# Performance work log

Measured on AMD Instinct MI355X. Metric: run time of the kernel, lower is better.

## Reference

```python
import jax, jax.numpy as jnp
import numpy as np

B, S, D, H = 4, 1024, 1024, 16
HD = D // H
EPS = 1e-5


def setup_inputs() -> dict:
    key = jax.random.key(0)
    ks = jax.random.split(key, 12)
    sc = 0.02
    return {
        "x": jax.random.normal(ks[0], (B, S, D), jnp.float32),
        "WQ": jax.random.normal(ks[1], (D, D), jnp.float32) * sc,
        "WK": jax.random.normal(ks[2], (D, D), jnp.float32) * sc,
        "WV": jax.random.normal(ks[3], (D, D), jnp.float32) * sc,
        "Wo": jax.random.normal(ks[4], (D, D), jnp.float32) * sc,
        "bo": jnp.zeros((D,), jnp.float32),
        "W1": jax.random.normal(ks[5], (D, 4 * D), jnp.float32) * sc,
        "b1": jnp.zeros((4 * D,), jnp.float32),
        "W2": jax.random.normal(ks[6], (4 * D, D), jnp.float32) * sc,
        "b2": jnp.zeros((D,), jnp.float32),
        "ln1_s": jnp.ones((D,), jnp.float32),
        "ln1_b": jnp.zeros((D,), jnp.float32),
        "ln2_s": jnp.ones((D,), jnp.float32),
        "ln2_b": jnp.zeros((D,), jnp.float32),
    }


def _layernorm(x, scale, shift):
    mean = jnp.mean(x, axis=-1, keepdims=True)
    var = jnp.mean((x - mean) ** 2, axis=-1, keepdims=True)  # unbiased=False
    return scale * ((x - mean) / jnp.sqrt(var + EPS)) + shift


def _gelu(x):
    c = jnp.sqrt(2.0 / jnp.pi).astype(x.dtype)
    return 0.5 * x * (1.0 + jnp.tanh(c * (x + 0.044715 * x ** 3)))


def reference(x, WQ, WK, WV, Wo, bo, W1, b1, W2, b2, ln1_s, ln1_b, ln2_s, ln2_b):
    b, s, d = x.shape
    # --- attention sub-block (pre-norm) ---
    h = _layernorm(x, ln1_s, ln1_b)
    q = (h @ WQ).reshape(b, s, H, HD).transpose(0, 2, 1, 3)  # [B,H,S,HD]
    k = (h @ WK).reshape(b, s, H, HD).transpose(0, 2, 1, 3)
    v = (h @ WV).reshape(b, s, H, HD).transpose(0, 2, 1, 3)
    scores = jnp.einsum("bhqd,bhkd->bhqk", q, k)
    causal = jnp.triu(jnp.ones((s, s), dtype=bool), k=1)
    scores = jnp.where(causal, -jnp.inf, scores)
    attn = jax.nn.softmax(scores / jnp.sqrt(jnp.float32(HD)), axis=-1)
    ctx = jnp.einsum("bhqk,bhkd->bhqd", attn, v)
    ctx = ctx.transpose(0, 2, 1, 3).reshape(b, s, d)
    x = x + (ctx @ Wo + bo)
    # --- FF sub-block (pre-norm) ---
    h = _layernorm(x, ln2_s, ln2_b)
    h = _gelu(h @ W1 + b1)
    return x + (h @ W2 + b2)
```

## Files before the change

### kernel.cpp

```cpp
#include <hip/hip_runtime.h>
#include <hip/hip_bf16.h>

#define DIM   1024
#define NHEAD 16
#define HDIM  64
#define BATCH 4
#define SEQ   1024
#define MTOT  (BATCH*SEQ)
#define DFF   (4*DIM)
#define LDQ   3072

typedef _Float16 f16x8 __attribute__((ext_vector_type(8)));
typedef _Float16 f16x4 __attribute__((ext_vector_type(4)));
typedef float    f32x4 __attribute__((ext_vector_type(4)));

__device__ __forceinline__ float geluf(float x) {
    float x3 = x * x * x;
    return 0.5f * x * (1.0f + tanhf(0.7978845608028654f * (x + 0.044715f * x3)));
}

__device__ __forceinline__ int swz_off(int row, int slot) {
    return row * 128 + ((slot ^ (row & 7)) << 4);
}
__device__ __forceinline__ f16x8 ldsfrag(const _Float16* s, int row, int slot) {
    return *(const f16x8*)((const char*)s + swz_off(row, slot));
}

template <int NCHUNK>
__device__ __forceinline__ void stage_async(const _Float16* __restrict__ g, int ld,
                                            _Float16* s, int w, int lane) {
    int r_in = lane >> 3;
    int sslot = lane & 7;
    int lslot = sslot ^ r_in;
#pragma unroll
    for (int q = 0; q < NCHUNK; ++q) {
        int chunk = w * NCHUNK + q;
        int row = chunk * 8 + r_in;
        const _Float16* gp = g + (size_t)row * ld + lslot * 8;
        _Float16* sp = s + chunk * 512;
        __builtin_amdgcn_global_load_lds(
            (const __attribute__((address_space(1))) void*)gp,
            (__attribute__((address_space(3))) void*)sp, 16, 0, 0);
    }
}

__global__ __launch_bounds__(256) void k_tcvt(const float* __restrict__ src,
                                              _Float16* __restrict__ dst,
                                              int K, int N) {
    __shared__ float tile[32][33];
    int n0 = blockIdx.x * 32, k0 = blockIdx.y * 32;
    int tx = threadIdx.x, ty = threadIdx.y;
#pragma unroll
    for (int i = 0; i < 32; i += 8)
        tile[ty + i][tx] = src[(size_t)(k0 + ty + i) * N + (n0 + tx)];
    __syncthreads();
#pragma unroll
    for (int i = 0; i < 32; i += 8)
        dst[(size_t)(n0 + ty + i) * K + (k0 + tx)] = (_Float16)tile[tx][ty + i];
}

__global__ __launch_bounds__(256) void k_tcvt3(const float* __restrict__ s0,
                                               const float* __restrict__ s1,
                                               const float* __restrict__ s2,
                                               _Float16* __restrict__ dst) {
    __shared__ float tile[32][33];
    const float* src = blockIdx.z == 0 ? s0 : (blockIdx.z == 1 ? s1 : s2);
    _Float16* d = dst + (size_t)blockIdx.z * (1024 * 1024);
    int n0 = blockIdx.x * 32, k0 = blockIdx.y * 32;
    int tx = threadIdx.x, ty = threadIdx.y;
#pragma unroll
    for (int i = 0; i < 32; i += 8)
        tile[ty + i][tx] = src[(size_t)(k0 + ty + i) * 1024 + (n0 + tx)];
    __syncthreads();
#pragma unroll
    for (int i = 0; i < 32; i += 8)
        d[(size_t)(n0 + ty + i) * 1024 + (k0 + tx)] = (_Float16)tile[tx][ty + i];
}

__global__ __launch_bounds__(256) void k_ln(const float* __restrict__ x,
                                            const float* __restrict__ sc,
                                            const float* __restrict__ sh,
                                            _Float16* __restrict__ out) {
    int row = blockIdx.x;
    int t = threadIdx.x;
    float4 v = ((const float4*)(x + (size_t)row * DIM))[t];
    float sum = v.x + v.y + v.z + v.w;
    float sq  = v.x * v.x + v.y * v.y + v.z * v.z + v.w * v.w;
#pragma unroll
    for (int m = 1; m < 64; m <<= 1) {
        sum += __shfl_xor(sum, m);
        sq  += __shfl_xor(sq, m);
    }
    __shared__ float rs[4], rq[4];
    int w = t >> 6;
    if ((t & 63) == 0) { rs[w] = sum; rq[w] = sq; }
    __syncthreads();
    sum = rs[0] + rs[1] + rs[2] + rs[3];
    sq  = rq[0] + rq[1] + rq[2] + rq[3];
    float mean = sum * (1.0f / DIM);
    float var  = sq * (1.0f / DIM) - mean * mean;
    float rstd = rsqrtf(var + 1e-5f);
    float4 s4 = ((const float4*)sc)[t];
    float4 b4 = ((const float4*)sh)[t];
    f16x4 o;
    o[0] = (_Float16)(s4.x * ((v.x - mean) * rstd) + b4.x);
    o[1] = (_Float16)(s4.y * ((v.y - mean) * rstd) + b4.y);
    o[2] = (_Float16)(s4.z * ((v.z - mean) * rstd) + b4.z);
    o[3] = (_Float16)(s4.w * ((v.w - mean) * rstd) + b4.w);
    ((f16x4*)(out + (size_t)row * DIM))[t] = o;
}

template <int EPI>
__global__ __launch_bounds__(256) void k_gemm(const _Float16* __restrict__ A,
                                              const _Float16* __restrict__ BT,
                                              int M, int N, int K,
                                              _Float16* __restrict__ Ch,
                                              const float* __restrict__ bias) {
    __shared__ _Float16 As[128 * 64];
    __shared__ _Float16 Bs[128 * 64];
    int t = threadIdx.x;
    int m0 = blockIdx.y * 128, n0 = blockIdx.x * 128;
    int lane = t & 63, w = t >> 6;
    int wm = (w >> 1) * 64, wn = (w & 1) * 64;
    int lr = lane & 15, lg = lane >> 4;
    f32x4 acc[4][4];
#pragma unroll
    for (int i = 0; i < 4; ++i)
#pragma unroll
        for (int j = 0; j < 4; ++j) acc[i][j] = (f32x4){0.f, 0.f, 0.f, 0.f};

    const _Float16* Ag = A  + (size_t)m0 * K;
    const _Float16* Bg = BT + (size_t)n0 * K;
    for (int k0 = 0; k0 < K; k0 += 64) {
        stage_async<4>(Ag + k0, K, As, w, lane);
        stage_async<4>(Bg + k0, K, Bs, w, lane);
        __syncthreads();
#pragma unroll
        for (int kk = 0; kk < 2; ++kk) {
            f16x8 a[4], b[4];
#pragma unroll
            for (int i = 0; i < 4; ++i) a[i] = ldsfrag(As, wm + i * 16 + lr, kk * 4 + lg);
#pragma unroll
            for (int j = 0; j < 4; ++j) b[j] = ldsfrag(Bs, wn + j * 16 + lr, kk * 4 + lg);
#pragma unroll
            for (int i = 0; i < 4; ++i)
#pragma unroll
                for (int j = 0; j < 4; ++j)
                    acc[i][j] = __builtin_amdgcn_mfma_f32_16x16x32_f16(a[i], b[j], acc[i][j], 0, 0, 0);
        }
        __syncthreads();
    }
#pragma unroll
    for (int i = 0; i < 4; ++i) {
#pragma unroll
        for (int j = 0; j < 4; ++j) {
            int row = m0 + wm + i * 16 + lg * 4;
            int col = n0 + wn + j * 16 + lr;
#pragma unroll
            for (int r = 0; r < 4; ++r) {
                float v = acc[i][j][r];
                size_t idx = (size_t)(row + r) * N + col;
                if constexpr (EPI == 0) Ch[idx] = (_Float16)v;
                else                    Ch[idx] = (_Float16)geluf(v + bias[col]);
            }
        }
    }
}

__global__ __launch_bounds__(256) void k_gemm64(const _Float16* __restrict__ A,
                                                const _Float16* __restrict__ BT,
                                                int M, int N, int K,
                                                float* __restrict__ Cf,
                                                const float* __restrict__ bias,
                                                const float* __restrict__ resid) {
    __shared__ _Float16 As[128 * 64];
    __shared__ _Float16 Bs[64 * 64];
    int t = threadIdx.x;
    int m0 = blockIdx.y * 128, n0 = blockIdx.x * 64;
    int lane = t & 63, w = t >> 6;
    int wm = w * 32;
    int lr = lane & 15, lg = lane >> 4;
    f32x4 acc[2][4];
#pragma unroll
    for (int i = 0; i < 2; ++i)
#pragma unroll
        for (int j = 0; j < 4; ++j) acc[i][j] = (f32x4){0.f, 0.f, 0.f, 0.f};

    const _Float16* Ag = A  + (size_t)m0 * K;
    const _Float16* Bg = BT + (size_t)n0 * K;
    for (int k0 = 0; k0 < K; k0 += 64) {
        stage_async<4>(Ag + k0, K, As, w, lane);
        stage_async<2>(Bg + k0, K, Bs, w, lane);
        __syncthreads();
#pragma unroll
        for (int kk = 0; kk < 2; ++kk) {
            f16x8 a[2], b[4];
#pragma unroll
            for (int i = 0; i < 2; ++i) a[i] = ldsfrag(As, wm + i * 16 + lr, kk * 4 + lg);
#pragma unroll
            for (int j = 0; j < 4; ++j) b[j] = ldsfrag(Bs, j * 16 + lr, kk * 4 + lg);
#pragma unroll
            for (int i = 0; i < 2; ++i)
#pragma unroll
                for (int j = 0; j < 4; ++j)
                    acc[i][j] = __builtin_amdgcn_mfma_f32_16x16x32_f16(a[i], b[j], acc[i][j], 0, 0, 0);
        }
        __syncthreads();
    }
#pragma unroll
    for (int i = 0; i < 2; ++i) {
#pragma unroll
        for (int j = 0; j < 4; ++j) {
            int row = m0 + wm + i * 16 + lg * 4;
            int col = n0 + j * 16 + lr;
#pragma unroll
            for (int r = 0; r < 4; ++r) {
                size_t idx = (size_t)(row + r) * N + col;
                Cf[idx] = acc[i][j][r] + bias[col] + resid[idx];
            }
        }
    }
}

__global__ __launch_bounds__(64) void k_attn(const _Float16* __restrict__ QKV,
                                             _Float16* __restrict__ Og) {
    __shared__ _Float16 Vt[64 * 64];
    __shared__ _Float16 Ps[32 * 64];
    int lane = threadIdx.x;
    int id = blockIdx.x;
    int bh = id & 63;
    int qt = (SEQ / 32 - 1) - (id >> 6);
    int h = bh & 15, b = bh >> 4;
    int q0 = qt * 32;
    int lr = lane & 15, lg = lane >> 4;
    size_t base = (size_t)b * SEQ;
    int cq = h * HDIM, ck = 1024 + h * HDIM, cv = 2048 + h * HDIM;

    f16x8 aq[2][2];
#pragma unroll
    for (int i = 0; i < 2; ++i)
#pragma unroll
        for (int kk = 0; kk < 2; ++kk) {
            f16x8 v = *(const f16x8*)(QKV + (base + q0 + i * 16 + lr) * LDQ + cq + kk * 32 + lg * 8);
#pragma unroll
            for (int e = 0; e < 8; ++e) v[e] = v[e] * (_Float16)0.125f;
            aq[i][kk] = v;
        }

    f32x4 cacc[2][4];
#pragma unroll
    for (int i = 0; i < 2; ++i)
#pragma unroll
        for (int j = 0; j < 4; ++j) cacc[i][j] = (f32x4){0.f, 0.f, 0.f, 0.f};
    float mrun[2][4], lrun[2][4];
#pragma unroll
    for (int i = 0; i < 2; ++i)
#pragma unroll
        for (int r = 0; r < 4; ++r) { mrun[i][r] = -1e30f; lrun[i][r] = 0.f; }

    int ntiles = q0 / 64 + 1;
    for (int kt = 0; kt < ntiles; ++kt) {
        int k0 = kt * 64;
        {
            const _Float16* vr = QKV + (base + k0 + lane) * LDQ + cv;
            int kslot = lane >> 3;
            int kb2 = (lane & 7) * 2;
#pragma unroll
            for (int part = 0; part < 8; ++part) {
                f16x8 v8 = *(const f16x8*)(vr + part * 8);
#pragma unroll
                for (int e = 0; e < 8; ++e) {
                    int d = part * 8 + e;
                    *(_Float16*)((char*)Vt + d * 128 + ((kslot ^ (d & 7)) << 4) + kb2) = v8[e];
                }
            }
        }
        f32x4 sacc[2][4];
#pragma unroll
        for (int i = 0; i < 2; ++i)
#pragma unroll
            for (int j = 0; j < 4; ++j) sacc[i][j] = (f32x4){0.f, 0.f, 0.f, 0.f};
#pragma unroll
        for (int kk = 0; kk < 2; ++kk) {
            f16x8 bk[4];
#pragma unroll
            for (int j = 0; j < 4; ++j)
                bk[j] = *(const f16x8*)(QKV + (base + k0 + j * 16 + lr) * LDQ + ck + kk * 32 + lg * 8);
            __builtin_amdgcn_s_setprio(1);
#pragma unroll
            for (int i = 0; i < 2; ++i)
#pragma unroll
                for (int j = 0; j < 4; ++j)
                    sacc[i][j] = __builtin_amdgcn_mfma_f32_16x16x32_f16(aq[i][kk], bk[j], sacc[i][j], 0, 0, 0);
            __builtin_amdgcn_s_setprio(0);
        }
        if (kt == ntiles - 1) {
#pragma unroll
            for (int i = 0; i < 2; ++i)
#pragma unroll
                for (int j = 0; j < 4; ++j)
#pragma unroll
                    for (int r = 0; r < 4; ++r) {
                        int qq = q0 + i * 16 + lg * 4 + r;
                        int kc = k0 + j * 16 + lr;
                        if (kc > qq) sacc[i][j][r] = -1e30f;
                    }
        }
#pragma unroll
        for (int i = 0; i < 2; ++i) {
            float mn[4], al[4];
#pragma unroll
            for (int r = 0; r < 4; ++r) {
                float tm = fmaxf(fmaxf(sacc[i][0][r], sacc[i][1][r]),
                                 fmaxf(sacc[i][2][r], sacc[i][3][r]));
#pragma unroll
                for (int msk = 1; msk < 16; msk <<= 1) tm = fmaxf(tm, __shfl_xor(tm, msk));
                float m2 = fmaxf(mrun[i][r], tm);
                al[r] = __expf(mrun[i][r] - m2);
                mrun[i][r] = m2;
                mn[r] = m2;
            }
#pragma unroll
            for (int jd = 0; jd < 4; ++jd)
#pragma unroll
                for (int r = 0; r < 4; ++r) cacc[i][jd][r] *= al[r];
#pragma unroll
            for (int r = 0; r < 4; ++r) {
                float ps = 0.f;
#pragma unroll
                for (int j = 0; j < 4; ++j) {
                    float p = __expf(sacc[i][j][r] - mn[r]);
                    sacc[i][j][r] = p;
                    ps += p;
                }
#pragma unroll
                for (int msk = 1; msk < 16; msk <<= 1) ps += __shfl_xor(ps, msk);
                lrun[i][r] = lrun[i][r] * al[r] + ps;
            }
        }
#pragma unroll
        for (int i = 0; i < 2; ++i)
#pragma unroll
            for (int j = 0; j < 4; ++j) {
                int kc = j * 16 + lr;
                int ks = kc >> 3;
                int kb = (kc & 7) * 2;
#pragma unroll
                for (int r = 0; r < 4; ++r) {
                    int qq = i * 16 + lg * 4 + r;
                    *(_Float16*)((char*)Ps + qq * 128 + ((ks ^ (qq & 7)) << 4) + kb) =
                        (_Float16)sacc[i][j][r];
                }
            }
#pragma unroll
        for (int kk = 0; kk < 2; ++kk) {
            f16x8 pa[2], bv[4];
#pragma unroll
            for (int i = 0; i < 2; ++i)   pa[i]  = ldsfrag(Ps, i * 16 + lr,  kk * 4 + lg);
#pragma unroll
            for (int jd = 0; jd < 4; ++jd) bv[jd] = ldsfrag(Vt, jd * 16 + lr, kk * 4 + lg);
            __builtin_amdgcn_s_setprio(1);
#pragma unroll
            for (int i = 0; i < 2; ++i)
#pragma unroll
                for (int jd = 0; jd < 4; ++jd)
                    cacc[i][jd] = __builtin_amdgcn_mfma_f32_16x16x32_f16(pa[i], bv[jd], cacc[i][jd], 0, 0, 0);
            __builtin_amdgcn_s_setprio(0);
        }
    }
#pragma unroll
    for (int i = 0; i < 2; ++i)
#pragma unroll
        for (int jd = 0; jd < 4; ++jd)
#pragma unroll
            for (int r = 0; r < 4; ++r) {
                int qq = q0 + i * 16 + lg * 4 + r;
                int d = h * HDIM + jd * 16 + lr;
                Og[(base + qq) * DIM + d] = (_Float16)(cacc[i][jd][r] / lrun[i][r]);
            }
}

extern "C" void kernel_launch(void* const* d_in, const int* in_sizes, int n_in,
                              void* d_out, int out_size, void* d_ws, size_t ws_size,
                              hipStream_t stream) {
    const float* x    = (const float*)d_in[0];
    const float* WQ   = (const float*)d_in[1];
    const float* WK   = (const float*)d_in[2];
    const float* WV   = (const float*)d_in[3];
    const float* Wo   = (const float*)d_in[4];
    const float* bo   = (const float*)d_in[5];
    const float* W1   = (const float*)d_in[6];
    const float* b1   = (const float*)d_in[7];
    const float* W2   = (const float*)d_in[8];
    const float* b2   = (const float*)d_in[9];
    const float* ln1s = (const float*)d_in[10];
    const float* ln1b = (const float*)d_in[11];
    const float* ln2s = (const float*)d_in[12];
    const float* ln2b = (const float*)d_in[13];
    float* out = (float*)d_out;
    char* ws = (char*)d_ws;
    const size_t MB = 1024 * 1024;
    _Float16* WTqkv = (_Float16*)(ws + 0 * MB);
    _Float16* WTo   = (_Float16*)(ws + 6 * MB);
    _Float16* WT1   = (_Float16*)(ws + 8 * MB);
    _Float16* WT2   = (_Float16*)(ws + 16 * MB);
    _Float16* h1    = (_Float16*)(ws + 24 * MB);
    _Float16* qkvb  = (_Float16*)(ws + 32 * MB);
    _Float16* ctx   = (_Float16*)(ws + 56 * MB);
    _Float16* h2    = (_Float16*)(ws + 64 * MB);
    _Float16* ff1   = (_Float16*)(ws + 72 * MB);
    float*    x2    = (float*)   (ws + 104 * MB);

    dim3 tb(32, 8);
    k_tcvt3<<<dim3(32, 32, 3), tb, 0, stream>>>(WQ, WK, WV, WTqkv);
    k_tcvt<<<dim3(32, 32), tb, 0, stream>>>(Wo, WTo, 1024, 1024);
    k_tcvt<<<dim3(128, 32), tb, 0, stream>>>(W1, WT1, 1024, 4096);
    k_tcvt<<<dim3(32, 128), tb, 0, stream>>>(W2, WT2, 4096, 1024);

    k_ln<<<MTOT, 256, 0, stream>>>(x, ln1s, ln1b, h1);

    k_gemm<0><<<dim3(24, 32), 256, 0, stream>>>(h1, WTqkv, MTOT, LDQ, DIM, qkvb, nullptr);

    k_attn<<<dim3(2048), 64, 0, stream>>>(qkvb, ctx);

    k_gemm64<<<dim3(16, 32), 256, 0, stream>>>(ctx, WTo, MTOT, DIM, DIM, x2, bo, x);

    k_ln<<<MTOT, 256, 0, stream>>>(x2, ln2s, ln2b, h2);

    k_gemm<1><<<dim3(32, 32), 256, 0, stream>>>(h2, WT1, MTOT, DFF, DIM, ff1, b1);

    k_gemm64<<<dim3(16, 32), 256, 0, stream>>>(ff1, WT2, MTOT, DIM, DFF, out, b2, x2);
}
```

Baseline: 258.5 us.

## Double-buffer GEMM LDS tiles, raise MFMA priority, use exp-based GELU

Both GEMM kernels now keep two LDS buffers, so the async load of the next K-tile is issued before the MFMAs on the current tile run, and only one barrier remains per iteration. The aim is to hide global-to-LDS latency behind matrix math. s_setprio raises wave priority around the MFMA block. GELU is rewritten as x*sigmoid(2z), using __expf and a hardware reciprocal instead of tanhf. The cost is double the LDS per block, which may lower occupancy, plus slightly reduced GELU precision.

```diff
diff --git a/kernel.cpp b/kernel.cpp
--- a/kernel.cpp
+++ b/kernel.cpp
@@ -15,8 +15,8 @@
 typedef float    f32x4 __attribute__((ext_vector_type(4)));
 
 __device__ __forceinline__ float geluf(float x) {
-    float x3 = x * x * x;
-    return 0.5f * x * (1.0f + tanhf(0.7978845608028654f * (x + 0.044715f * x3)));
+    float z2 = 1.5957691216057308f * (x + 0.044715f * x * x * x);
+    return x * __builtin_amdgcn_rcpf(1.0f + __expf(-z2));
 }
 
 __device__ __forceinline__ int swz_off(int row, int slot) {
@@ -116,8 +116,8 @@
                                               int M, int N, int K,
                                               _Float16* __restrict__ Ch,
                                               const float* __restrict__ bias) {
-    __shared__ _Float16 As[128 * 64];
-    __shared__ _Float16 Bs[128 * 64];
+    __shared__ _Float16 As[2][128 * 64];
+    __shared__ _Float16 Bs[2][128 * 64];
     int t = threadIdx.x;
     int m0 = blockIdx.y * 128, n0 = blockIdx.x * 128;
     int lane = t & 63, w = t >> 6;
@@ -131,22 +131,30 @@
 
     const _Float16* Ag = A  + (size_t)m0 * K;
     const _Float16* Bg = BT + (size_t)n0 * K;
-    for (int k0 = 0; k0 < K; k0 += 64) {
-        stage_async<4>(Ag + k0, K, As, w, lane);
-        stage_async<4>(Bg + k0, K, Bs, w, lane);
-        __syncthreads();
+    int nt = K / 64;
+    stage_async<4>(Ag, K, As[0], w, lane);
+    stage_async<4>(Bg, K, Bs[0], w, lane);
+    __syncthreads();
+    for (int tt = 0; tt < nt; ++tt) {
+        int cur = tt & 1, nxt = cur ^ 1;
+        if (tt + 1 < nt) {
+            stage_async<4>(Ag + (tt + 1) * 64, K, As[nxt], w, lane);
+            stage_async<4>(Bg + (tt + 1) * 64, K, Bs[nxt], w, lane);
+        }
 #pragma unroll
         for (int kk = 0; kk < 2; ++kk) {
             f16x8 a[4], b[4];
 #pragma unroll
-            for (int i = 0; i < 4; ++i) a[i] = ldsfrag(As, wm + i * 16 + lr, kk * 4 + lg);
-#pragma unroll
-            for (int j = 0; j < 4; ++j) b[j] = ldsfrag(Bs, wn + j * 16 + lr, kk * 4 + lg);
+            for (int i = 0; i < 4; ++i) a[i] = ldsfrag(As[cur], wm + i * 16 + lr, kk * 4 + lg);
+#pragma unroll
+            for (int j = 0; j < 4; ++j) b[j] = ldsfrag(Bs[cur], wn + j * 16 + lr, kk * 4 + lg);
+            __builtin_amdgcn_s_setprio(1);
 #pragma unroll
             for (int i = 0; i < 4; ++i)
 #pragma unroll
                 for (int j = 0; j < 4; ++j)
                     acc[i][j] = __builtin_amdgcn_mfma_f32_16x16x32_f16(a[i], b[j], acc[i][j], 0, 0, 0);
+            __builtin_amdgcn_s_setprio(0);
         }
         __syncthreads();
     }
@@ -173,8 +181,8 @@
                                                 float* __restrict__ Cf,
                                                 const float* __restrict__ bias,
                                                 const float* __restrict__ resid) {
-    __shared__ _Float16 As[128 * 64];
-    __shared__ _Float16 Bs[64 * 64];
+    __shared__ _Float16 As[2][128 * 64];
+    __shared__ _Float16 Bs[2][64 * 64];
     int t = threadIdx.x;
     int m0 = blockIdx.y * 128, n0 = blockIdx.x * 64;
     int lane = t & 63, w = t >> 6;
@@ -188,22 +196,30 @@
 
     const _Float16* Ag = A  + (size_t)m0 * K;
     const _Float16* Bg = BT + (size_t)n0 * K;
-    for (int k0 = 0; k0 < K; k0 += 64) {
-        stage_async<4>(Ag + k0, K, As, w, lane);
-        stage_async<2>(Bg + k0, K, Bs, w, lane);
-        __syncthreads();
+    int nt = K / 64;
+    stage_async<4>(Ag, K, As[0], w, lane);
+    stage_async<2>(Bg, K, Bs[0], w, lane);
+    __syncthreads();
+    for (int tt = 0; tt < nt; ++tt) {
+        int cur = tt & 1, nxt = cur ^ 1;
+        if (tt + 1 < nt) {
+            stage_async<4>(Ag + (tt + 1) * 64, K, As[nxt], w, lane);
+            stage_async<2>(Bg + (tt + 1) * 64, K, Bs[nxt], w, lane);
+        }
 #pragma unroll
         for (int kk = 0; kk < 2; ++kk) {
             f16x8 a[2], b[4];
 #pragma unroll
-            for (int i = 0; i < 2; ++i) a[i] = ldsfrag(As, wm + i * 16 + lr, kk * 4 + lg);
-#pragma unroll
-            for (int j = 0; j < 4; ++j) b[j] = ldsfrag(Bs, j * 16 + lr, kk * 4 + lg);
+            for (int i = 0; i < 2; ++i) a[i] = ldsfrag(As[cur], wm + i * 16 + lr, kk * 4 + lg);
+#pragma unroll
+            for (int j = 0; j < 4; ++j) b[j] = ldsfrag(Bs[cur], j * 16 + lr, kk * 4 + lg);
+            __builtin_amdgcn_s_setprio(1);
 #pragma unroll
             for (int i = 0; i < 2; ++i)
 #pragma unroll
                 for (int j = 0; j < 4; ++j)
                     acc[i][j] = __builtin_amdgcn_mfma_f32_16x16x32_f16(a[i], b[j], acc[i][j], 0, 0, 0);
+            __builtin_amdgcn_s_setprio(0);
         }
         __syncthreads();
     }
```

Result: faster. 245.5 us (-5.0%).
